# Optimization experiments

Measured on AMD Instinct MI355X. Metric: run time of the kernel, lower is better.

## Reference

```python
import jax, jax.numpy as jnp
import numpy as np

DIM, E, K = 256, 8, 2
B, D, H, W = 1, 32, 32, 32
EPS = 1e-5


def setup_inputs() -> dict:
    key = jax.random.key(0)
    ks = jax.random.split(key, 16)
    nrm = lambda k, s, sc=0.02: jax.random.normal(k, s, jnp.float32) * sc
    def resblock_params(k):
        k1, k2, k3, k4 = jax.random.split(k, 4)
        return dict(
            c1w=nrm(k1, (DIM, DIM, 3, 3, 3)), c1b=jnp.zeros((DIM,), jnp.float32),
            g1=jax.random.uniform(k2, (DIM,), jnp.float32, 0.5, 1.5), be1=jnp.zeros((DIM,), jnp.float32),
            c2w=nrm(k3, (DIM, DIM, 3, 3, 3)), c2b=jnp.zeros((DIM,), jnp.float32),
            g2=jax.random.uniform(k4, (DIM,), jnp.float32, 0.5, 1.5), be2=jnp.zeros((DIM,), jnp.float32),
        )
    p1 = resblock_params(ks[5])
    p2 = resblock_params(ks[6])
    return {
        "x": jax.random.normal(ks[0], (B, DIM, D, H, W), jnp.float32),
        "wg": nrm(ks[1], (DIM, E)),
        "w1": nrm(ks[2], (E, DIM, DIM)), "b1": jnp.zeros((E, DIM), jnp.float32),
        "w2": nrm(ks[3], (E, DIM, DIM)), "b2": jnp.zeros((E, DIM), jnp.float32),
        "r1_c1w": p1["c1w"], "r1_c1b": p1["c1b"], "r1_g1": p1["g1"], "r1_be1": p1["be1"],
        "r1_c2w": p1["c2w"], "r1_c2b": p1["c2b"], "r1_g2": p1["g2"], "r1_be2": p1["be2"],
        "r2_c1w": p2["c1w"], "r2_c1b": p2["c1b"], "r2_g1": p2["g1"], "r2_be1": p2["be1"],
        "r2_c2w": p2["c2w"], "r2_c2b": p2["c2b"], "r2_g2": p2["g2"], "r2_be2": p2["be2"],
        "c8w": nrm(ks[4], (DIM, DIM, 1, 1, 1)), "c8b": jnp.zeros((DIM,), jnp.float32),
    }


def conv3d(x, w, b, pad):
    y = jax.lax.conv_general_dilated(
        x, w, window_strides=(1, 1, 1), padding=[(pad, pad)] * 3,
        dimension_numbers=("NCDHW", "OIDHW", "NCDHW"))
    return y + b[None, :, None, None, None]


def batchnorm(x, g, b):
    m = x.mean(axis=(0, 2, 3, 4), keepdims=True)
    v = x.var(axis=(0, 2, 3, 4), keepdims=True)
    return g[None, :, None, None, None] * (x - m) * jax.lax.rsqrt(v + EPS) + b[None, :, None, None, None]


def unet_res_block(x, c1w, c1b, g1, be1, c2w, c2b, g2, be2):
    out = jax.nn.leaky_relu(batchnorm(conv3d(x, c1w, c1b, 1), g1, be1), 0.01)
    out = batchnorm(conv3d(out, c2w, c2b, 1), g2, be2)
    return jax.nn.leaky_relu(out + x, 0.01)  # identity shortcut (in==out ch, stride 1)


def mom_block(x, wg, w1, b1, w2, b2):
    Bb, C, Dd, Hh, Ww = x.shape
    tokens = x.transpose(0, 2, 3, 4, 1).reshape(-1, C)  # [T, C]
    T = tokens.shape[0]
    probs = jax.nn.softmax(tokens @ wg, axis=-1)          # [T, E]
    vals, idx = jax.lax.top_k(probs, K)                   # [T, K]
    wts = vals / vals.sum(-1, keepdims=True)
    gates = jnp.zeros((T, E), probs.dtype).at[jnp.arange(T)[:, None], idx].set(wts)
    # dense expert MLPs (math-equivalent to gather/dispatch/combine)
    h = jax.nn.gelu(jnp.einsum("tc,ech->eth", tokens, w1) + b1[:, None, :])
    eo = jnp.einsum("eth,ehc->etc", h, w2) + b2[:, None, :]
    moe = jnp.einsum("te,etc->tc", gates, eo)             # [T, C]
    # switch-style load-balancing auxiliary loss
    density = (gates > 0).astype(probs.dtype).mean(0)     # fraction of tokens per expert
    density_proxy = probs.mean(0)
    aux = (density * density_proxy).sum() * E
    out = x + moe.reshape(Bb, Dd, Hh, Ww, C).transpose(0, 4, 1, 2, 3)
    return out, aux


def reference(x, wg, w1, b1, w2, b2,
              r1_c1w, r1_c1b, r1_g1, r1_be1, r1_c2w, r1_c2b, r1_g2, r1_be2,
              r2_c1w, r2_c1b, r2_g1, r2_be1, r2_c2w, r2_c2b, r2_g2, r2_be2,
              c8w, c8b):
    xm, aux = mom_block(x, wg, w1, b1, w2, b2)
    res = unet_res_block(xm, r1_c1w, r1_c1b, r1_g1, r1_be1, r1_c2w, r1_c2b, r1_g2, r1_be2)
    res = unet_res_block(res, r2_c1w, r2_c1b, r2_g1, r2_be1, r2_c2w, r2_c2b, r2_g2, r2_be2)
    out = xm + conv3d(res, c8w, c8b, 0)  # Dropout3d is identity at eval
    return out, aux
```

## Files before the change

kernel.cpp:

```cpp
#include <hip/hip_runtime.h>
#include <stdint.h>

typedef __attribute__((ext_vector_type(8))) short short8;
typedef __attribute__((ext_vector_type(4))) float f32x4;
typedef unsigned short u16;
typedef unsigned int u32;
typedef unsigned long long u64;

#define WS_TOK   0ull
#define WS_XT    16777216ull
#define WS_XMCT  50331648ull
#define WS_GATES 83886080ull
#define WS_H     84934656ull
#define WS_MOE   101711872ull
#define WS_P1    135266304ull
#define WS_P2    155389952ull
#define WS_Y     175513600ull
#define WS_R2    209068032ull
#define WS_WRB   225845248ull
#define WS_W1P   240001024ull
#define WS_W2P   241049600ull
#define WS_C8P   242098176ull
#define WS_PART  242229248ull
#define WS_SF    243277824ull
#define WS_AUXP  243279872ull

#define WS_PERM  (WS_H + 0x00000ull)
#define WS_TBL   (WS_H + 0x60000ull)
#define WS_META  (WS_H + 0x70000ull)
#define WS_BCNT  (WS_H + 0x80000ull)
#define WS_BOFF  (WS_H + 0x90000ull)
#define WS_SEL   (WS_H + 0x100000ull)

__device__ __forceinline__ u16 f2bf(float f) {
  u32 x = __float_as_uint(f);
  u32 r = x + 0x7fffu + ((x >> 16) & 1u);
  return (u16)(r >> 16);
}

__global__ void trans_in_k(const float* __restrict__ x, float* __restrict__ xt,
                           u16* __restrict__ tok) {
  __shared__ float ld[64][65];
  int tt = blockIdx.x, cc = blockIdx.y, tid = threadIdx.x;
#pragma unroll
  for (int k = 0; k < 16; ++k) {
    int idx = tid + k * 256;
    int cl = idx >> 6, j = idx & 63;
    ld[cl][j] = x[(size_t)(cc * 64 + cl) * 32768 + tt * 64 + j];
  }
  __syncthreads();
#pragma unroll
  for (int k = 0; k < 16; ++k) {
    int idx = tid + k * 256;
    int tl = idx >> 6, cl = idx & 63;
    float v = ld[cl][tl];
    size_t o = (size_t)(tt * 64 + tl) * 256 + cc * 64 + cl;
    xt[o] = v;
    tok[o] = f2bf(v);
  }
}

__global__ void pack_rb_k(const float* __restrict__ w0, const float* __restrict__ w1,
                          const float* __restrict__ w2, const float* __restrict__ w3,
                          u16* __restrict__ out) {
  __shared__ float ld[6912];
  int conv = blockIdx.x >> 8, blk = blockIdx.x & 255, tid = threadIdx.x;
  const float* src = conv == 0 ? w0 : conv == 1 ? w1 : conv == 2 ? w2 : w3;
  size_t base = (size_t)blk * 256 * 27;
#pragma unroll
  for (int k = 0; k < 27; ++k) ld[tid + k * 256] = src[base + tid + k * 256];
  __syncthreads();
  u16* dst = out + (size_t)conv * 27 * 65536;
  int n = blk * 256 + tid;
#pragma unroll
  for (int tap = 0; tap < 27; ++tap)
    dst[(size_t)tap * 65536 + n] = f2bf(ld[tid * 27 + tap]);
}

__global__ void pack_tr_k(const float* __restrict__ w1, const float* __restrict__ w2,
                          u16* __restrict__ w1p, u16* __restrict__ w2p) {
  __shared__ float ld[64][65];
  int m = blockIdx.y, tile = blockIdx.x, tid = threadIdx.x;
  const float* src = (m < 8) ? (w1 + (size_t)m * 65536) : (w2 + (size_t)(m - 8) * 65536);
  u16* dst = (m < 8) ? (w1p + (size_t)m * 65536) : (w2p + (size_t)(m - 8) * 65536);
  int r0 = (tile >> 2) * 64, c0 = (tile & 3) * 64;
#pragma unroll
  for (int k = 0; k < 16; ++k) {
    int idx = tid + k * 256;
    int rr = idx >> 6, cc = idx & 63;
    ld[rr][cc] = src[(size_t)(r0 + rr) * 256 + c0 + cc];
  }
  __syncthreads();
#pragma unroll
  for (int k = 0; k < 16; ++k) {
    int idx = tid + k * 256;
    int cc = idx >> 6, rr = idx & 63;
    dst[(size_t)(c0 + cc) * 256 + r0 + rr] = f2bf(ld[rr][cc]);
  }
}

__global__ void cvt_k(const float* __restrict__ in, u16* __restrict__ out, int n) {
  int i = blockIdx.x * 256 + threadIdx.x;
  if (i < n) out[i] = f2bf(in[i]);
}

__global__ void halo_k(u16* __restrict__ P1, u16* __restrict__ P2) {
  int gid = blockIdx.x * 256 + threadIdx.x;
  int r = gid >> 5, o = (gid & 31) << 3;
  if (r >= 39304) return;
  int d = r / 1156, rem = r - d * 1156, h = rem / 34, w = rem - h * 34;
  if (d >= 1 && d <= 32 && h >= 1 && h <= 32 && w >= 1 && w <= 32) return;
  uint4 z = {0u, 0u, 0u, 0u};
  *(uint4*)(P1 + (size_t)r * 256 + o) = z;
  *(uint4*)(P2 + (size_t)r * 256 + o) = z;
}

__global__ void gate_k(const float* __restrict__ xt, const float* __restrict__ wg,
                       float* __restrict__ gw, u32* __restrict__ sel,
                       u32* __restrict__ blk_cnt, float* __restrict__ auxp) {
  __shared__ float wgs[2048];
  __shared__ float ax[4][16];
  __shared__ u32 bc[4][8];
  int tid = threadIdx.x;
#pragma unroll
  for (int k = 0; k < 8; ++k) wgs[tid + k * 256] = wg[tid + k * 256];
  __syncthreads();
  int t = blockIdx.x * 256 + tid;
  int lane = tid & 63, wv = tid >> 6;
  float l[8] = {0, 0, 0, 0, 0, 0, 0, 0};
  const float* xr = xt + (size_t)t * 256;
  for (int c = 0; c < 256; c += 4) {
    float4 xv = *(const float4*)(xr + c);
#pragma unroll
    for (int e = 0; e < 8; ++e)
      l[e] += xv.x * wgs[c * 8 + e] + xv.y * wgs[(c + 1) * 8 + e] +
              xv.z * wgs[(c + 2) * 8 + e] + xv.w * wgs[(c + 3) * 8 + e];
  }
  float mx = l[0];
#pragma unroll
  for (int e = 1; e < 8; ++e) mx = fmaxf(mx, l[e]);
  float p[8], sum = 0.f;
#pragma unroll
  for (int e = 0; e < 8; ++e) { p[e] = __expf(l[e] - mx); sum += p[e]; }
  float inv = 1.0f / sum;
#pragma unroll
  for (int e = 0; e < 8; ++e) p[e] *= inv;
  int i0 = 0; float v0 = p[0];
#pragma unroll
  for (int e = 1; e < 8; ++e) if (p[e] > v0) { v0 = p[e]; i0 = e; }
  int i1 = -1; float v1 = -1.0f;
#pragma unroll
  for (int e = 0; e < 8; ++e) if (e != i0 && p[e] > v1) { v1 = p[e]; i1 = e; }
  float wsum = v0 + v1;
  gw[t * 2] = v0 / wsum;
  gw[t * 2 + 1] = v1 / wsum;
  sel[t] = (u32)i0 | ((u32)i1 << 4);
  u64 mm[8];
#pragma unroll
  for (int e = 0; e < 8; ++e) mm[e] = __ballot(i0 == e || i1 == e);
  if (lane == 0) {
#pragma unroll
    for (int e = 0; e < 8; ++e) bc[wv][e] = (u32)__popcll(mm[e]);
  }
#pragma unroll
  for (int e = 0; e < 8; ++e) {
    float ps = p[e];
    float cn = (e == i0 || e == i1) ? 1.0f : 0.0f;
    for (int o = 32; o; o >>= 1) { ps += __shfl_down(ps, o); cn += __shfl_down(cn, o); }
    if (lane == 0) { ax[wv][e] = ps; ax[wv][8 + e] = cn; }
  }
  __syncthreads();
  if (tid < 16)
    auxp[blockIdx.x * 16 + tid] = ax[0][tid] + ax[1][tid] + ax[2][tid] + ax[3][tid];
  if (tid < 8)
    blk_cnt[blockIdx.x * 8 + tid] = bc[0][tid] + bc[1][tid] + bc[2][tid] + bc[3][tid];
}

__global__ void aux_k(const float* __restrict__ auxp, float* __restrict__ out) {
  __shared__ float s[16];
  int i = threadIdx.x;
  if (i < 16) {
    float a = 0;
    for (int b = 0; b < 128; ++b) a += auxp[b * 16 + i];
    s[i] = a;
  }
  __syncthreads();
  if (i == 0) {
    float r = 0;
    for (int e = 0; e < 8; ++e)
      r += (s[8 + e] * (1.0f / 32768.0f)) * (s[e] * (1.0f / 32768.0f));
    out[0] = r * 8.0f;
  }
}

__global__ void scan_k(const u32* __restrict__ blk_cnt, u32* __restrict__ blkoff,
                       u32* __restrict__ tbl, u32* __restrict__ meta,
                       u32* __restrict__ perm) {
  __shared__ u32 tot[8], base[8], nck[8], cbase[8];
  int tid = threadIdx.x;
  if (tid < 8) {
    u32 run = 0;
    for (int b = 0; b < 128; ++b) {
      blkoff[b * 8 + tid] = run;
      run += blk_cnt[b * 8 + tid];
    }
    tot[tid] = run;
  }
  __syncthreads();
  if (tid == 0) {
    u32 acc = 0, c = 0;
    for (int e = 0; e < 8; ++e) {
      base[e] = acc;
      u32 nc = (tot[e] + 127) >> 7;
      nck[e] = nc;
      cbase[e] = c;
      acc += nc << 7;
      c += nc;
    }
    meta[0] = c;
  }
  __syncthreads();
  for (int i = tid; i < 1024; i += 256) blkoff[i] += base[i & 7];
  if (tid < 8) {
    for (u32 k = 0; k < nck[tid]; ++k)
      tbl[cbase[tid] + k] = ((base[tid] + (k << 7)) << 4) | (u32)tid;
    for (u32 sl = base[tid] + tot[tid]; sl < base[tid] + (nck[tid] << 7); ++sl)
      perm[sl] = 0;
  }
}

__global__ void scatter_k(const u32* __restrict__ sel, const u32* __restrict__ blkoff,
                          u32* __restrict__ perm, u32* __restrict__ tpos) {
  __shared__ u32 wcnt[4][8];
  int tid = threadIdx.x, b = blockIdx.x;
  int lane = tid & 63, wv = tid >> 6;
  int t = b * 256 + tid;
  u32 s = sel[t];
  int i0 = s & 15, i1 = (s >> 4) & 15;
  u64 mm[8];
#pragma unroll
  for (int e = 0; e < 8; ++e) mm[e] = __ballot(i0 == e || i1 == e);
  if (lane == 0) {
#pragma unroll
    for (int e = 0; e < 8; ++e) wcnt[wv][e] = (u32)__popcll(mm[e]);
  }
  __syncthreads();
  u64 lt = (1ull << lane) - 1ull;
#pragma unroll
  for (int e = 0; e < 8; ++e) {
    bool is0 = (i0 == e), is1 = (i1 == e);
    if (is0 || is1) {
      u32 woff = 0;
#pragma unroll
      for (int w = 0; w < 4; ++w)
        if (w < wv) woff += wcnt[w][e];
      u32 pos = blkoff[b * 8 + e] + woff + (u32)__popcll(mm[e] & lt);
      perm[pos] = (u32)t;
      tpos[t * 2 + (is0 ? 0 : 1)] = pos;
    }
  }
}

__global__ __launch_bounds__(512, 2) void moe_gemm_k(
    const u16* __restrict__ tok, const u32* __restrict__ perm,
    const u32* __restrict__ tbl, const u32* __restrict__ meta,
    const u16* __restrict__ w1p, const u16* __restrict__ w2p,
    const float* __restrict__ b1, const float* __restrict__ b2,
    u16* __restrict__ eo) {
  __shared__ __attribute__((aligned(16))) unsigned char smem[163840];
  const int bid = blockIdx.x;
  if ((u32)bid >= meta[0]) return;
  const u32 ent = tbl[bid];
  const int e = (int)(ent & 15u);
  const int slot0 = (int)(ent >> 4);
  const int tid = threadIdx.x;
  const int lane = tid & 63;
  const int wv = tid >> 6;
  const int wr = (wv >> 2) * 64;
  const int wc = (wv & 3) * 64;
  const int fq = lane >> 4, fr = lane & 15;
  const u16* w1e = w1p + e * 65536;
  const u16* w2e = w2p + e * 65536;

#pragma unroll
  for (int it = 0; it < 8; ++it) {
    int s = tid + it * 512;
    int r = s >> 5, seg = s & 31;
    int cole = ((seg >> 3) << 6) + (((seg & 7) ^ (r & 7)) << 3);
    u32 rowtok = perm[slot0 + r];
    __builtin_amdgcn_global_load_lds(
        (const __attribute__((address_space(1))) u32*)(tok + (size_t)rowtok * 256 + cole),
        (__attribute__((address_space(3))) u32*)(smem + s * 16), 16, 0, 0);
  }

  f32x4 acc1[4][4];
#pragma unroll
  for (int mc = 0; mc < 4; ++mc)
#pragma unroll
    for (int nt = 0; nt < 4; ++nt) acc1[mc][nt] = (f32x4){0.f, 0.f, 0.f, 0.f};

#pragma unroll 1
  for (int kc = 0; kc < 4; ++kc) {
#pragma unroll
    for (int it = 0; it < 4; ++it) {
      int s = tid + it * 512;
      int r = s >> 3;
      int sub = (s & 7) ^ (r & 7);
      __builtin_amdgcn_global_load_lds(
          (const __attribute__((address_space(1))) u32*)(w1e + (size_t)r * 256 + kc * 64 + sub * 8),
          (__attribute__((address_space(3))) u32*)(smem + 65536 + s * 16), 16, 0, 0);
    }
    __syncthreads();
#pragma unroll
    for (int khf = 0; khf < 2; ++khf) {
      short8 af1[4], bt[4];
#pragma unroll
      for (int mc = 0; mc < 4; ++mc) {
        int row = wc + mc * 16 + fr;
        int p = (khf * 4 + fq) ^ (row & 7);
        af1[mc] = *(const short8*)(smem + 65536 + row * 128 + p * 16);
      }
#pragma unroll
      for (int nt = 0; nt < 4; ++nt) {
        int row = wr + nt * 16 + fr;
        int p = (khf * 4 + fq) ^ (row & 7);
        bt[nt] = *(const short8*)(smem + row * 512 + kc * 128 + p * 16);
      }
#pragma unroll
      for (int mc = 0; mc < 4; ++mc)
#pragma unroll
        for (int nt = 0; nt < 4; ++nt)
          acc1[mc][nt] = __builtin_amdgcn_mfma_f32_16x16x32_bf16(af1[mc], bt[nt], acc1[mc][nt], 0, 0, 0);
    }
    __syncthreads();
  }

#pragma unroll
  for (int mc = 0; mc < 4; ++mc) {
    int k0 = wc + mc * 16 + fq * 4;
    float4 bv = *(const float4*)(b1 + e * 256 + k0);
#pragma unroll
    for (int nt = 0; nt < 4; ++nt) {
      int t = wr + nt * 16 + fr;
      u64 pk = 0;
#pragma unroll
      for (int j = 0; j < 4; ++j) {
        float v = acc1[mc][nt][j] + ((const float*)&bv)[j];
        float u = 1.5957691216057308f * (v + 0.044715f * v * v * v);
        float g = v / (1.0f + __expf(-u));
        pk |= (u64)f2bf(g) << (16 * j);
      }
      *(u64*)(smem + 98304 + t * 512 + ((k0 * 2) ^ ((t & 7) << 4))) = pk;
    }
  }

  f32x4 acc2[4][4];
#pragma unroll
  for (int m = 0; m < 4; ++m)
#pragma unroll
    for (int n = 0; n < 4; ++n) acc2[m][n] = (f32x4){0.f, 0.f, 0.f, 0.f};

#pragma unroll 1
  for (int kc = 0; kc < 4; ++kc) {
#pragma unroll
    for (int it = 0; it < 4; ++it) {
      int s = tid + it * 512;
      int r = s >> 3;
      int sub = (s & 7) ^ (r & 7);
      __builtin_amdgcn_global_load_lds(
          (const __attribute__((address_space(1))) u32*)(w2e + (size_t)r * 256 + kc * 64 + sub * 8),
          (__attribute__((address_space(3))) u32*)(smem + 65536 + s * 16), 16, 0, 0);
    }
    __syncthreads();
#pragma unroll
    for (int khf = 0; khf < 2; ++khf) {
      short8 af[4], bb[4];
#pragma unroll
      for (int m = 0; m < 4; ++m) {
        int row = wr + m * 16 + fr;
        int col = (kc * 128 + (khf * 4 + fq) * 16) ^ ((row & 7) << 4);
        af[m] = *(const short8*)(smem + 98304 + row * 512 + col);
      }
#pragma unroll
      for (int n = 0; n < 4; ++n) {
        int row = wc + n * 16 + fr;
        int p = (khf * 4 + fq) ^ (row & 7);
        bb[n] = *(const short8*)(smem + 65536 + row * 128 + p * 16);
      }
#pragma unroll
      for (int m = 0; m < 4; ++m)
#pragma unroll
        for (int n = 0; n < 4; ++n)
          acc2[m][n] = __builtin_amdgcn_mfma_f32_16x16x32_bf16(af[m], bb[n], acc2[m][n], 0, 0, 0);
    }
    __syncthreads();
  }

  float bs2[4];
#pragma unroll
  for (int n = 0; n < 4; ++n) bs2[n] = b2[e * 256 + wc + n * 16 + fr];
#pragma unroll
  for (int m = 0; m < 4; ++m)
#pragma unroll
    for (int j = 0; j < 4; ++j) {
      int rowslot = slot0 + wr + m * 16 + fq * 4 + j;
      u16* er = eo + (size_t)rowslot * 256 + wc;
#pragma unroll
      for (int n = 0; n < 4; ++n) er[n * 16 + fr] = f2bf(acc2[m][n][j] + bs2[n]);
    }
}

__global__ void combine_k(float* __restrict__ xt, const u16* __restrict__ eo,
                          const float* __restrict__ gw, const u32* __restrict__ tpos,
                          float* __restrict__ xmct, u16* __restrict__ pad) {
  __shared__ float ld[64][65];
  __shared__ u32 pp[64][2];
  __shared__ float gg[64][2];
  int tt = blockIdx.x, cc = blockIdx.y, tid = threadIdx.x;
  if (tid < 128) {
    int tl = tid >> 1, s = tid & 1;
    int t = tt * 64 + tl;
    pp[tl][s] = tpos[t * 2 + s];
    gg[tl][s] = gw[t * 2 + s];
  }
  __syncthreads();
#pragma unroll
  for (int k = 0; k < 16; ++k) {
    int idx = tid + k * 256;
    int tl = idx >> 6, cl = idx & 63;
    int c = cc * 64 + cl;
    size_t o = (size_t)(tt * 64 + tl) * 256 + c;
    float e0 = __uint_as_float((u32)eo[(size_t)pp[tl][0] * 256 + c] << 16);
    float e1 = __uint_as_float((u32)eo[(size_t)pp[tl][1] * 256 + c] << 16);
    float v = xt[o] + gg[tl][0] * e0 + gg[tl][1] * e1;
    xt[o] = v;
    ld[tl][cl] = v;
    int t = tt * 64 + tl;
    int d = t >> 10, h = (t >> 5) & 31, w = t & 31;
    int prow = (d + 1) * 1156 + (h + 1) * 34 + (w + 1);
    pad[(size_t)prow * 256 + c] = f2bf(v);
  }
  __syncthreads();
#pragma unroll
  for (int k = 0; k < 16; ++k) {
    int idx = tid + k * 256;
    int cl = idx >> 6, tl = idx & 63;
    xmct[(size_t)(cc * 64 + cl) * 32768 + tt * 64 + tl] = ld[tl][cl];
  }
}

template <int MODE>
__global__ __launch_bounds__(256, 2) void gemm_k(
    const u16* __restrict__ A, const u16* __restrict__ Bw,
    const float* __restrict__ bias, float* __restrict__ outF,
    const float* __restrict__ xmct, float* __restrict__ part) {
  __shared__ __attribute__((aligned(16))) unsigned char smem[32768];
  const int tid = threadIdx.x;
  const int bx = blockIdx.x;
  const int ttile = (MODE == 0) ? ((bx & 7) * 32 + (bx >> 3)) : bx;
  const int ctile = blockIdx.y;
  const int lane = tid & 63;
  const int wv = tid >> 6;
  const int wr = (wv >> 1) << 6;
  const int wc = (wv & 1) << 6;
  const int fq = lane >> 4;
  const int fr = lane & 15;

  int aoff[4], boff[4];
#pragma unroll
  for (int it = 0; it < 4; ++it) {
    int s = tid + it * 256;
    int r = s >> 3;
    int lsg = (s & 7) ^ (r & 7);
    if (MODE == 0) {
      int dd = ttile >> 3;
      int h0 = (ttile & 7) << 2;
      int base = dd * 1156 + (h0 + (r >> 5)) * 34 + (r & 31);
      aoff[it] = base * 256 + lsg * 8;
    } else {
      aoff[it] = (ttile * 128 + r) * 256 + lsg * 8;
    }
    boff[it] = (ctile * 128 + r) * 256 + lsg * 8;
  }

  f32x4 acc[4][4];
#pragma unroll
  for (int m = 0; m < 4; ++m)
#pragma unroll
    for (int n = 0; n < 4; ++n) acc[m][n] = (f32x4){0.f, 0.f, 0.f, 0.f};

  const int nTap = (MODE == 0) ? 27 : 1;
#pragma unroll 1
  for (int tap = 0; tap < nTap; ++tap) {
    int atap = 0, btap = 0;
    if (MODE == 0) {
      atap = ((tap / 9) * 1156 + ((tap / 3) % 3) * 34 + (tap % 3)) * 256;
      btap = tap * 65536;
    }
#pragma unroll 1
    for (int kc = 0; kc < 4; ++kc) {
      const u16* Ak = A + atap + kc * 64;
      const u16* Bk = Bw + btap + kc * 64;
#pragma unroll
      for (int it = 0; it < 4; ++it) {
        __builtin_amdgcn_global_load_lds(
            (const __attribute__((address_space(1))) u32*)(Ak + aoff[it]),
            (__attribute__((address_space(3))) u32*)(smem + (tid + it * 256) * 16),
            16, 0, 0);
        __builtin_amdgcn_global_load_lds(
            (const __attribute__((address_space(1))) u32*)(Bk + boff[it]),
            (__attribute__((address_space(3))) u32*)(smem + 16384 + (tid + it * 256) * 16),
            16, 0, 0);
      }
      __syncthreads();
#pragma unroll
      for (int khf = 0; khf < 2; ++khf) {
        short8 af[4], bb[4];
#pragma unroll
        for (int m = 0; m < 4; ++m) {
          int row = wr + m * 16 + fr;
          int p = (khf * 4 + fq) ^ (row & 7);
          af[m] = *(const short8*)(smem + row * 128 + p * 16);
        }
#pragma unroll
        for (int n = 0; n < 4; ++n) {
          int row = wc + n * 16 + fr;
          int p = (khf * 4 + fq) ^ (row & 7);
          bb[n] = *(const short8*)(smem + 16384 + row * 128 + p * 16);
        }
#pragma unroll
        for (int m = 0; m < 4; ++m)
#pragma unroll
          for (int n = 0; n < 4; ++n)
            acc[m][n] = __builtin_amdgcn_mfma_f32_16x16x32_bf16(af[m], bb[n], acc[m][n], 0, 0, 0);
      }
      __syncthreads();
    }
  }

  float bs[4];
#pragma unroll
  for (int n = 0; n < 4; ++n) bs[n] = bias[ctile * 128 + wc + n * 16 + fr];

  if (MODE == 3) {
#pragma unroll
    for (int m = 0; m < 4; ++m) {
      int trow = ttile * 128 + wr + m * 16 + fq * 4;
#pragma unroll
      for (int n = 0; n < 4; ++n) {
        int oc = ctile * 128 + wc + n * 16 + fr;
        size_t o = (size_t)oc * 32768 + trow;
        float4 xv = *(const float4*)(xmct + o);
        float4 w;
        w.x = acc[m][n][0] + bs[n] + xv.x;
        w.y = acc[m][n][1] + bs[n] + xv.y;
        w.z = acc[m][n][2] + bs[n] + xv.z;
        w.w = acc[m][n][3] + bs[n] + xv.w;
        *(float4*)(outF + o) = w;
      }
    }
  } else {
    float sn[4] = {0, 0, 0, 0}, qn[4] = {0, 0, 0, 0};
#pragma unroll
    for (int m = 0; m < 4; ++m) {
#pragma unroll
      for (int j = 0; j < 4; ++j) {
        int t = ttile * 128 + wr + m * 16 + fq * 4 + j;
        float* yr = outF + (size_t)t * 256 + ctile * 128 + wc;
#pragma unroll
        for (int n = 0; n < 4; ++n) {
          float v = acc[m][n][j] + bs[n];
          yr[n * 16 + fr] = v;
          sn[n] += v;
          qn[n] += v * v;
        }
      }
    }
#pragma unroll
    for (int n = 0; n < 4; ++n) {
      float s = sn[n], q = qn[n];
      s += __shfl_xor(s, 16); s += __shfl_xor(s, 32);
      q += __shfl_xor(q, 16); q += __shfl_xor(q, 32);
      if (lane < 16) {
        int pi = (ttile * 2 + (wv >> 1)) * 256 + ctile * 128 + wc + n * 16 + fr;
        part[pi] = s;
        part[131072 + pi] = q;
      }
    }
  }
}

__global__ void stats2_k(const float* __restrict__ part, const float* __restrict__ g,
                         const float* __restrict__ be, float* __restrict__ sf) {
  __shared__ float sred[4][256], qred[4][256];
  int tid = threadIdx.x;
  int c = tid & 255, qd = tid >> 8;
  float s = 0, q = 0;
  for (int b = qd * 128; b < qd * 128 + 128; ++b) {
    s += part[b * 256 + c];
    q += part[131072 + b * 256 + c];
  }
  sred[qd][c] = s;
  qred[qd][c] = q;
  __syncthreads();
  if (qd == 0) {
    s = sred[0][c] + sred[1][c] + sred[2][c] + sred[3][c];
    q = qred[0][c] + qred[1][c] + qred[2][c] + qred[3][c];
    float mean = s * (1.0f / 32768.0f);
    float var = q * (1.0f / 32768.0f) - mean * mean;
    float a = g[c] * rsqrtf(var + 1e-5f);
    sf[c] = a;
    sf[256 + c] = be[c] - mean * a;
  }
}

template <int V>
__global__ void bn_k(const float* __restrict__ y, const float* __restrict__ sf,
                     const float* __restrict__ skip, u16* __restrict__ pad,
                     float* __restrict__ f32o, u16* __restrict__ bfo) {
  int gid = blockIdx.x * 256 + threadIdx.x;
  int t = gid >> 5, c0 = (gid & 31) << 3;
  size_t base = (size_t)t * 256 + c0;
  float v[8];
  const float4* yp = (const float4*)(y + base);
  float4 y0 = yp[0], y1 = yp[1];
  const float4* ap = (const float4*)(sf + c0);
  float4 a0 = ap[0], a1 = ap[1];
  const float4* shp = (const float4*)(sf + 256 + c0);
  float4 s0 = shp[0], s1 = shp[1];
  v[0] = a0.x * y0.x + s0.x; v[1] = a0.y * y0.y + s0.y;
  v[2] = a0.z * y0.z + s0.z; v[3] = a0.w * y0.w + s0.w;
  v[4] = a1.x * y1.x + s1.x; v[5] = a1.y * y1.y + s1.y;
  v[6] = a1.z * y1.z + s1.z; v[7] = a1.w * y1.w + s1.w;
  if (V >= 1) {
    const float4* kp = (const float4*)(skip + base);
    float4 k0 = kp[0], k1 = kp[1];
    v[0] += k0.x; v[1] += k0.y; v[2] += k0.z; v[3] += k0.w;
    v[4] += k1.x; v[5] += k1.y; v[6] += k1.z; v[7] += k1.w;
  }
#pragma unroll
  for (int i = 0; i < 8; ++i) v[i] = v[i] > 0.0f ? v[i] : 0.01f * v[i];
  if (V <= 1) {
    int d = t >> 10, h = (t >> 5) & 31, w = t & 31;
    int prow = (d + 1) * 1156 + (h + 1) * 34 + (w + 1);
    uint4 pk;
    pk.x = (u32)f2bf(v[0]) | ((u32)f2bf(v[1]) << 16);
    pk.y = (u32)f2bf(v[2]) | ((u32)f2bf(v[3]) << 16);
    pk.z = (u32)f2bf(v[4]) | ((u32)f2bf(v[5]) << 16);
    pk.w = (u32)f2bf(v[6]) | ((u32)f2bf(v[7]) << 16);
    *(uint4*)(pad + (size_t)prow * 256 + c0) = pk;
  }
  if (V == 1) {
    float4 o0 = {v[0], v[1], v[2], v[3]}, o1 = {v[4], v[5], v[6], v[7]};
    float4* fp = (float4*)(f32o + base);
    fp[0] = o0; fp[1] = o1;
  }
  if (V == 2) {
    uint4 pk;
    pk.x = (u32)f2bf(v[0]) | ((u32)f2bf(v[1]) << 16);
    pk.y = (u32)f2bf(v[2]) | ((u32)f2bf(v[3]) << 16);
    pk.z = (u32)f2bf(v[4]) | ((u32)f2bf(v[5]) << 16);
    pk.w = (u32)f2bf(v[6]) | ((u32)f2bf(v[7]) << 16);
    *(uint4*)(bfo + base) = pk;
  }
}

extern "C" void kernel_launch(void* const* d_in, const int* in_sizes, int n_in,
                              void* d_out, int out_size, void* d_ws, size_t ws_size,
                              hipStream_t stream) {
  (void)in_sizes; (void)n_in; (void)out_size; (void)ws_size;
  const float* x  = (const float*)d_in[0];
  const float* wg = (const float*)d_in[1];
  const float* w1 = (const float*)d_in[2];
  const float* b1 = (const float*)d_in[3];
  const float* w2 = (const float*)d_in[4];
  const float* b2 = (const float*)d_in[5];

  char* ws = (char*)d_ws;
  u16* tok    = (u16*)(ws + WS_TOK);
  float* xt   = (float*)(ws + WS_XT);
  float* xmct = (float*)(ws + WS_XMCT);
  float* gw   = (float*)(ws + WS_GATES);
  u32* tpos   = (u32*)(ws + WS_GATES + 0x80000ull);
  u32* perm   = (u32*)(ws + WS_PERM);
  u32* tbl    = (u32*)(ws + WS_TBL);
  u32* meta   = (u32*)(ws + WS_META);
  u32* bcnt   = (u32*)(ws + WS_BCNT);
  u32* boff   = (u32*)(ws + WS_BOFF);
  u32* selb   = (u32*)(ws + WS_SEL);
  u16* P1     = (u16*)(ws + WS_P1);
  u16* P2     = (u16*)(ws + WS_P2);
  float* ybuf = (float*)(ws + WS_Y);
  u16* eo     = (u16*)(ws + WS_Y);
  u16* r2b    = (u16*)(ws + WS_R2);
  u16* wrb    = (u16*)(ws + WS_WRB);
  u16* w1p    = (u16*)(ws + WS_W1P);
  u16* w2p    = (u16*)(ws + WS_W2P);
  u16* c8p    = (u16*)(ws + WS_C8P);
  float* part = (float*)(ws + WS_PART);
  float* sf   = (float*)(ws + WS_SF);
  float* auxp = (float*)(ws + WS_AUXP);
  float* outp = (float*)d_out;

  halo_k<<<4913, 256, 0, stream>>>(P1, P2);
  trans_in_k<<<dim3(512, 4), 256, 0, stream>>>(x, xt, tok);
  pack_rb_k<<<1024, 256, 0, stream>>>((const float*)d_in[6], (const float*)d_in[10],
                                      (const float*)d_in[14], (const float*)d_in[18], wrb);
  pack_tr_k<<<dim3(16, 16), 256, 0, stream>>>(w1, w2, w1p, w2p);
  cvt_k<<<256, 256, 0, stream>>>((const float*)d_in[22], c8p, 65536);

  gate_k<<<128, 256, 0, stream>>>(xt, wg, gw, selb, bcnt, auxp);
  scan_k<<<1, 256, 0, stream>>>(bcnt, boff, tbl, meta, perm);
  scatter_k<<<128, 256, 0, stream>>>(selb, boff, perm, tpos);
  moe_gemm_k<<<520, 512, 0, stream>>>(tok, perm, tbl, meta, w1p, w2p, b1, b2, eo);
  combine_k<<<dim3(512, 4), 256, 0, stream>>>(xt, eo, gw, tpos, xmct, P1);

  gemm_k<0><<<dim3(256, 2), 256, 0, stream>>>(P1, wrb + 0 * 1769472, (const float*)d_in[7],
                                              ybuf, nullptr, part);
  stats2_k<<<1, 1024, 0, stream>>>(part, (const float*)d_in[8], (const float*)d_in[9], sf);
  bn_k<0><<<4096, 256, 0, stream>>>(ybuf, sf, nullptr, P2, nullptr, nullptr);
  gemm_k<0><<<dim3(256, 2), 256, 0, stream>>>(P2, wrb + 1 * 1769472, (const float*)d_in[11],
                                              ybuf, nullptr, part);
  stats2_k<<<1, 1024, 0, stream>>>(part, (const float*)d_in[12], (const float*)d_in[13], sf);
  bn_k<1><<<4096, 256, 0, stream>>>(ybuf, sf, xt, P1, xt, nullptr);

  gemm_k<0><<<dim3(256, 2), 256, 0, stream>>>(P1, wrb + 2 * 1769472, (const float*)d_in[15],
                                              ybuf, nullptr, part);
  stats2_k<<<1, 1024, 0, stream>>>(part, (const float*)d_in[16], (const float*)d_in[17], sf);
  bn_k<0><<<4096, 256, 0, stream>>>(ybuf, sf, nullptr, P2, nullptr, nullptr);
  gemm_k<0><<<dim3(256, 2), 256, 0, stream>>>(P2, wrb + 3 * 1769472, (const float*)d_in[19],
                                              ybuf, nullptr, part);
  stats2_k<<<1, 1024, 0, stream>>>(part, (const float*)d_in[20], (const float*)d_in[21], sf);
  bn_k<2><<<4096, 256, 0, stream>>>(ybuf, sf, xt, nullptr, nullptr, r2b);

  gemm_k<3><<<dim3(256, 2), 256, 0, stream>>>(r2b, c8p, (const float*)d_in[23], outp,
                                              xmct, nullptr);
  aux_k<<<1, 64, 0, stream>>>(auxp, outp + 8388608);
}
```

Before: 718.3 us.

## Double-buffer LDS in GEMM kernel to overlap global loads with MFMA

```diff
diff --git a/kernel.cpp b/kernel.cpp
--- a/kernel.cpp
+++ b/kernel.cpp
@@ -12,7 +12,6 @@
 #define WS_XMCT  50331648ull
 #define WS_GATES 83886080ull
 #define WS_H     84934656ull
-#define WS_MOE   101711872ull
 #define WS_P1    135266304ull
 #define WS_P2    155389952ull
 #define WS_Y     175513600ull
@@ -454,7 +453,7 @@
     const u16* __restrict__ A, const u16* __restrict__ Bw,
     const float* __restrict__ bias, float* __restrict__ outF,
     const float* __restrict__ xmct, float* __restrict__ part) {
-  __shared__ __attribute__((aligned(16))) unsigned char smem[32768];
+  __shared__ __attribute__((aligned(16))) unsigned char smem[65536];
   const int tid = threadIdx.x;
   const int bx = blockIdx.x;
   const int ttile = (MODE == 0) ? ((bx & 7) * 32 + (bx >> 3)) : bx;
@@ -489,53 +488,68 @@
 #pragma unroll
     for (int n = 0; n < 4; ++n) acc[m][n] = (f32x4){0.f, 0.f, 0.f, 0.f};
 
-  const int nTap = (MODE == 0) ? 27 : 1;
-#pragma unroll 1
-  for (int tap = 0; tap < nTap; ++tap) {
+  const int nStep = (MODE == 0) ? 108 : 4;
+
+  auto stage = [&](int s, int buf) {
+    int tap = (MODE == 0) ? (s >> 2) : 0;
+    int kc = s & 3;
     int atap = 0, btap = 0;
     if (MODE == 0) {
       atap = ((tap / 9) * 1156 + ((tap / 3) % 3) * 34 + (tap % 3)) * 256;
       btap = tap * 65536;
     }
+    const u16* Ak = A + atap + kc * 64;
+    const u16* Bk = Bw + btap + kc * 64;
+    unsigned char* sb = smem + buf * 32768;
+#pragma unroll
+    for (int it = 0; it < 4; ++it) {
+      __builtin_amdgcn_global_load_lds(
+          (const __attribute__((address_space(1))) u32*)(Ak + aoff[it]),
+          (__attribute__((address_space(3))) u32*)(sb + (tid + it * 256) * 16),
+          16, 0, 0);
+      __builtin_amdgcn_global_load_lds(
+          (const __attribute__((address_space(1))) u32*)(Bk + boff[it]),
+          (__attribute__((address_space(3))) u32*)(sb + 16384 + (tid + it * 256) * 16),
+          16, 0, 0);
+    }
+  };
+
+  auto compute = [&](int buf) {
+    unsigned char* sb = smem + buf * 32768;
+#pragma unroll
+    for (int khf = 0; khf < 2; ++khf) {
+      short8 af[4], bb[4];
+#pragma unroll
+      for (int m = 0; m < 4; ++m) {
+        int row = wr + m * 16 + fr;
+        int p = (khf * 4 + fq) ^ (row & 7);
+        af[m] = *(const short8*)(sb + row * 128 + p * 16);
+      }
+#pragma unroll
+      for (int n = 0; n < 4; ++n) {
+        int row = wc + n * 16 + fr;
+        int p = (khf * 4 + fq) ^ (row & 7);
+        bb[n] = *(const short8*)(sb + 16384 + row * 128 + p * 16);
+      }
+#pragma unroll
+      for (int m = 0; m < 4; ++m)
+#pragma unroll
+        for (int n = 0; n < 4; ++n)
+          acc[m][n] = __builtin_amdgcn_mfma_f32_16x16x32_bf16(af[m], bb[n], acc[m][n], 0, 0, 0);
+    }
+  };
+
+  stage(0, 0);
+  asm volatile("s_waitcnt vmcnt(0)" ::: "memory");
+  __builtin_amdgcn_s_barrier();
+  int cur = 0;
 #pragma unroll 1
-    for (int kc = 0; kc < 4; ++kc) {
-      const u16* Ak = A + atap + kc * 64;
-      const u16* Bk = Bw + btap + kc * 64;
-#pragma unroll
-      for (int it = 0; it < 4; ++it) {
-        __builtin_amdgcn_global_load_lds(
-            (const __attribute__((address_space(1))) u32*)(Ak + aoff[it]),
-            (__attribute__((address_space(3))) u32*)(smem + (tid + it * 256) * 16),
-            16, 0, 0);
-        __builtin_amdgcn_global_load_lds(
-            (const __attribute__((address_space(1))) u32*)(Bk + boff[it]),
-            (__attribute__((address_space(3))) u32*)(smem + 16384 + (tid + it * 256) * 16),
-            16, 0, 0);
-      }
-      __syncthreads();
-#pragma unroll
-      for (int khf = 0; khf < 2; ++khf) {
-        short8 af[4], bb[4];
-#pragma unroll
-        for (int m = 0; m < 4; ++m) {
-          int row = wr + m * 16 + fr;
-          int p = (khf * 4 + fq) ^ (row & 7);
-          af[m] = *(const short8*)(smem + row * 128 + p * 16);
-        }
-#pragma unroll
-        for (int n = 0; n < 4; ++n) {
-          int row = wc + n * 16 + fr;
-          int p = (khf * 4 + fq) ^ (row & 7);
-          bb[n] = *(const short8*)(smem + 16384 + row * 128 + p * 16);
-        }
-#pragma unroll
-        for (int m = 0; m < 4; ++m)
-#pragma unroll
-          for (int n = 0; n < 4; ++n)
-            acc[m][n] = __builtin_amdgcn_mfma_f32_16x16x32_bf16(af[m], bb[n], acc[m][n], 0, 0, 0);
-      }
-      __syncthreads();
-    }
+  for (int s = 0; s < nStep; ++s) {
+    if (s + 1 < nStep) stage(s + 1, cur ^ 1);
+    compute(cur);
+    asm volatile("s_waitcnt vmcnt(0)" ::: "memory");
+    __builtin_amdgcn_s_barrier();
+    cur ^= 1;
   }
 
   float bs[4];
```

New measurement: 713.8 us. No clear change (-0.6%).
